# Optimization experiments

Measured on AMD Instinct MI355X. Metric: run time of the kernel, lower is better.

## Reference

```python
import jax, jax.numpy as jnp
from jax import lax
import numpy as np

IN, FC1, H = 12, 32, 16  # hard-coded dims from the module

def setup_inputs() -> dict:
    key = jax.random.key(0)
    ks = jax.random.split(key, 12)
    B, T = 4096, 512
    s = 0.1
    return {
        "x":   jax.random.normal(ks[0], (B, T, IN), dtype=jnp.float32),
        "h0":  jax.random.normal(ks[1], (1, B, H), dtype=jnp.float32),
        "c0":  jax.random.normal(ks[2], (1, B, H), dtype=jnp.float32),
        "W1":  jax.random.normal(ks[3], (FC1, IN), dtype=jnp.float32) * s,
        "b1":  jax.random.normal(ks[4], (FC1,), dtype=jnp.float32) * s,
        "W_ih": jax.random.normal(ks[5], (4 * H, FC1), dtype=jnp.float32) * s,
        "W_hh": jax.random.normal(ks[6], (4 * H, H), dtype=jnp.float32) * s,
        "b_ih": jax.random.normal(ks[7], (4 * H,), dtype=jnp.float32) * s,
        "b_hh": jax.random.normal(ks[8], (4 * H,), dtype=jnp.float32) * s,
        "W2":  jax.random.normal(ks[9], (1, H), dtype=jnp.float32) * s,
        "b2":  jax.random.normal(ks[10], (1,), dtype=jnp.float32) * s,
    }

def reference(x, h0, c0, W1, b1, W_ih, W_hh, b_ih, b_hh, W2, b2):
    # fc1 + ReLU: [B,T,12] -> [B,T,32]
    u = jnp.maximum(jnp.einsum('bti,fi->btf', x, W1) + b1, 0.0)
    # Precompute input contribution to all gates: [B,T,4H]
    xg = jnp.einsum('btf,gf->btg', u, W_ih) + (b_ih + b_hh)
    def step(carry, xg_t):
        ht, ct = carry  # [B,H]
        gates = xg_t + ht @ W_hh.T  # [B,4H]; PyTorch gate order i,f,g,o
        i, f, g, o = jnp.split(gates, 4, axis=-1)
        ct = jax.nn.sigmoid(f) * ct + jax.nn.sigmoid(i) * jnp.tanh(g)
        ht = jax.nn.sigmoid(o) * jnp.tanh(ct)
        return (ht, ct), None
    (hT, cT), _ = lax.scan(step, (h0[0], c0[0]), xg.transpose(1, 0, 2))
    # last_step of batch_first LSTM output == final hidden state hT
    out = jnp.tanh(hT @ W2.T + b2)  # [B,1]
    return out, hT[None], cT[None]
```

## Files before the change

kernel.cpp:

```cpp
#include <hip/hip_runtime.h>

typedef __fp16 f16;
typedef __attribute__((ext_vector_type(4))) __fp16 h16x4;
typedef __attribute__((ext_vector_type(4))) float f32x4;

__device__ __forceinline__ float sigm(float x) {
    return __builtin_amdgcn_rcpf(1.0f + __expf(-x));
}
__device__ __forceinline__ float tanh_fast(float x) {
    return 1.0f - 2.0f * __builtin_amdgcn_rcpf(1.0f + __expf(2.0f * x));
}
__device__ __forceinline__ h16x4 cvt4(float4 v) {
    h16x4 r; r[0] = (f16)v.x; r[1] = (f16)v.y; r[2] = (f16)v.z; r[3] = (f16)v.w;
    return r;
}
__device__ __forceinline__ h16x4 pack4(float a, float b, float c, float d) {
    auto p0 = __builtin_amdgcn_cvt_pkrtz(a, b);
    auto p1 = __builtin_amdgcn_cvt_pkrtz(c, d);
    uint2 u = make_uint2(__builtin_bit_cast(unsigned, p0),
                         __builtin_bit_cast(unsigned, p1));
    return __builtin_bit_cast(h16x4, u);
}
__device__ __forceinline__ float sel4(f32x4 v, bool q1, bool q2) {
    float a = q1 ? v[1] : v[0];
    float b = q1 ? v[3] : v[2];
    return q2 ? b : a;
}

__global__ __launch_bounds__(128) void reflex_fused(
    const float* __restrict__ x,
    const float* __restrict__ h0, const float* __restrict__ c0,
    const float* __restrict__ W1, const float* __restrict__ b1,
    const float* __restrict__ Wih, const float* __restrict__ Whh,
    const float* __restrict__ bih, const float* __restrict__ bhh,
    const float* __restrict__ W2, const float* __restrict__ b2,
    float* __restrict__ dout)
{
    const int tid = threadIdx.x;
    const int lane = tid & 63;
    const int m = lane & 15, hi = lane >> 4;
    const int b0 = blockIdx.x << 2;

    __shared__ uint2 xgl[2][1024];

    if (tid >= 64) {
        const int e = m & 3, q = m >> 2;
        const int b = b0 + e;
        h16x4 a1[2]; f32x4 c1[2];
#pragma unroll
        for (int nt = 0; nt < 2; ++nt) {
            float4 wv = make_float4(0.f, 0.f, 0.f, 0.f);
            if (hi < 3) wv = *(const float4*)(W1 + (nt * 16 + m) * 12 + 4 * hi);
            a1[nt] = cvt4(wv);
            float4 bv = *(const float4*)(b1 + nt * 16 + 4 * hi);
            c1[nt] = f32x4{bv.x, bv.y, bv.z, bv.w};
        }
        h16x4 a2[4][2];
#pragma unroll
        for (int G = 0; G < 4; ++G) {
            const int gr = G * 16 + m;
#pragma unroll
            for (int s = 0; s < 2; ++s)
                a2[G][s] = cvt4(*(const float4*)(Wih + gr * 32 + s * 16 + 4 * hi));
        }
        const int psA = q * 64 + hi * 16 + e;
        const int psB = (hi ^ q) << 2;
        const float* xrow = x + (size_t)b * 512 * 12 + 4 * hi;

        for (int F = 0; F < 32; ++F) {
            float4 bxp[4];
#pragma unroll
            for (int C = 0; C < 4; ++C)
                if (hi < 3)
                    bxp[C] = *(const float4*)(xrow + (F * 16 + C * 4 + q) * 12);
            uint2* wb = &xgl[F & 1][0];
#pragma unroll
            for (int C = 0; C < 4; ++C) {
                h16x4 bx = {0, 0, 0, 0};
                if (hi < 3) bx = cvt4(bxp[C]);
                f32x4 d0 = __builtin_amdgcn_mfma_f32_16x16x16f16(a1[0], bx, c1[0], 0, 0, 0);
                f32x4 d1 = __builtin_amdgcn_mfma_f32_16x16x16f16(a1[1], bx, c1[1], 0, 0, 0);
                h16x4 u0 = pack4(fmaxf(d0[0], 0.f), fmaxf(d0[1], 0.f),
                                 fmaxf(d0[2], 0.f), fmaxf(d0[3], 0.f));
                h16x4 u1 = pack4(fmaxf(d1[0], 0.f), fmaxf(d1[1], 0.f),
                                 fmaxf(d1[2], 0.f), fmaxf(d1[3], 0.f));
                f32x4 z4 = {0.f, 0.f, 0.f, 0.f};
                f32x4 A0 = __builtin_amdgcn_mfma_f32_16x16x16f16(a2[0][0], u0, z4, 0, 0, 0);
                f32x4 A1 = __builtin_amdgcn_mfma_f32_16x16x16f16(a2[1][0], u0, z4, 0, 0, 0);
                f32x4 A2 = __builtin_amdgcn_mfma_f32_16x16x16f16(a2[2][0], u0, z4, 0, 0, 0);
                f32x4 A3 = __builtin_amdgcn_mfma_f32_16x16x16f16(a2[3][0], u0, z4, 0, 0, 0);
                A0 = __builtin_amdgcn_mfma_f32_16x16x16f16(a2[0][1], u1, A0, 0, 0, 0);
                A1 = __builtin_amdgcn_mfma_f32_16x16x16f16(a2[1][1], u1, A1, 0, 0, 0);
                A2 = __builtin_amdgcn_mfma_f32_16x16x16f16(a2[2][1], u1, A2, 0, 0, 0);
                A3 = __builtin_amdgcn_mfma_f32_16x16x16f16(a2[3][1], u1, A3, 0, 0, 0);
#pragma unroll
                for (int r = 0; r < 4; ++r) {
                    uint2 w_;
                    auto w0 = __builtin_amdgcn_cvt_pkrtz(A0[r], A1[r]);
                    auto w1 = __builtin_amdgcn_cvt_pkrtz(A2[r], A3[r]);
                    w_.x = __builtin_bit_cast(unsigned, w0);
                    w_.y = __builtin_bit_cast(unsigned, w1);
                    wb[psA + C * 256 + (psB ^ (r << 2))] = w_;
                }
            }
            __syncthreads();
        }
    } else {
        const int e = m >> 2, q = m & 3;
        const int b = b0 + e;
        const bool q1 = (q & 1) != 0, q2 = (q & 2) != 0;

        h16x4 ar[4]; f32x4 cb[4];
#pragma unroll
        for (int G = 0; G < 4; ++G) {
            const int gr = G * 16 + m;
            ar[G] = cvt4(*(const float4*)(Whh + gr * 16 + 4 * hi));
            float4 bi = *(const float4*)(bih + G * 16 + 4 * hi);
            float4 bh = *(const float4*)(bhh + G * 16 + 4 * hi);
            cb[G] = f32x4{bi.x + bh.x, bi.y + bh.y, bi.z + bh.z, bi.w + bh.w};
        }
        h16x4 hf = cvt4(*(const float4*)(h0 + b * 16 + 4 * hi));
        float cs = c0[b * 16 + 4 * hi + q];
        float hn = 0.f;
        int va[4];
#pragma unroll
        for (int j = 0; j < 4; ++j) va[j] = hi * 16 + ((q ^ hi ^ j) << 2) + e;

#define STEP(TT, QC) do {                                                      \
    f32x4 di = __builtin_amdgcn_mfma_f32_16x16x16f16(ar[0], hf, cb[0],0,0,0);  \
    f32x4 df = __builtin_amdgcn_mfma_f32_16x16x16f16(ar[1], hf, cb[1],0,0,0);  \
    f32x4 dg = __builtin_amdgcn_mfma_f32_16x16x16f16(ar[2], hf, cb[2],0,0,0);  \
    f32x4 dq = __builtin_amdgcn_mfma_f32_16x16x16f16(ar[3], hf, cb[3],0,0,0);  \
    h16x4 gx = __builtin_bit_cast(h16x4, QC);                                  \
    if ((TT) < 14) QC = bcur[((TT) + 2) * 64 + va[((TT) + 2) & 3]];            \
    float gg = sel4(dg, q1, q2) + (float)gx[2];                                \
    float gi = sel4(di, q1, q2) + (float)gx[0];                                \
    float gf = sel4(df, q1, q2) + (float)gx[1];                                \
    float go = sel4(dq, q1, q2) + (float)gx[3];                                \
    float tg = tanh_fast(gg);                                                  \
    cs = fmaf(sigm(gf), cs, sigm(gi) * tg);                                    \
    hn = sigm(go) * tanh_fast(cs);                                             \
    int hnb = __builtin_bit_cast(int, hn);                                     \
    float j0 = __builtin_bit_cast(float,                                       \
        __builtin_amdgcn_mov_dpp(hnb, 0x00, 0xF, 0xF, true));                  \
    float j1 = __builtin_bit_cast(float,                                       \
        __builtin_amdgcn_mov_dpp(hnb, 0x55, 0xF, 0xF, true));                  \
    float j2 = __builtin_bit_cast(float,                                       \
        __builtin_amdgcn_mov_dpp(hnb, 0xAA, 0xF, 0xF, true));                  \
    float j3 = __builtin_bit_cast(float,                                       \
        __builtin_amdgcn_mov_dpp(hnb, 0xFF, 0xF, 0xF, true));                  \
    hf = pack4(j0, j1, j2, j3);                                                \
} while (0)

        __builtin_amdgcn_s_setprio(1);
        for (int T = 0; T < 32; ++T) {
            __syncthreads();
            const uint2* bcur = &xgl[T & 1][0];
            uint2 qA = bcur[va[0]];
            uint2 qB = bcur[64 + va[1]];
            STEP(0, qA);  STEP(1, qB);
            STEP(2, qA);  STEP(3, qB);
            STEP(4, qA);  STEP(5, qB);
            STEP(6, qA);  STEP(7, qB);
            STEP(8, qA);  STEP(9, qB);
            STEP(10, qA); STEP(11, qB);
            STEP(12, qA); STEP(13, qB);
            STEP(14, qA); STEP(15, qB);
        }
        __builtin_amdgcn_s_setprio(0);
#undef STEP

        dout[4096 + b * 16 + 4 * hi + q]         = hn;
        dout[4096 + 65536 + b * 16 + 4 * hi + q] = cs;
        float p = hn * W2[4 * hi + q];
        p += __shfl_xor(p, 1);
        p += __shfl_xor(p, 2);
        p += __shfl_xor(p, 16);
        p += __shfl_xor(p, 32);
        if (hi == 0 && q == 0) dout[b0 + e] = tanh_fast(p + b2[0]);
    }
}

extern "C" void kernel_launch(void* const* d_in, const int* in_sizes, int n_in,
                              void* d_out, int out_size, void* d_ws, size_t ws_size,
                              hipStream_t stream)
{
    const float* x   = (const float*)d_in[0];
    const float* h0  = (const float*)d_in[1];
    const float* c0  = (const float*)d_in[2];
    const float* W1  = (const float*)d_in[3];
    const float* b1  = (const float*)d_in[4];
    const float* Wih = (const float*)d_in[5];
    const float* Whh = (const float*)d_in[6];
    const float* bih = (const float*)d_in[7];
    const float* bhh = (const float*)d_in[8];
    const float* W2  = (const float*)d_in[9];
    const float* b2  = (const float*)d_in[10];
    float* out = (float*)d_out;

    reflex_fused<<<dim3(1024), dim3(128), 0, stream>>>(
        x, h0, c0, W1, b1, Wih, Whh, bih, bhh, W2, b2, out);
}
```

Baseline: 102.2 us.

## Stage fp32 gate pre-activations in MFMA layout to feed recurrence accumulators directly

```diff
diff --git a/kernel.cpp b/kernel.cpp
--- a/kernel.cpp
+++ b/kernel.cpp
@@ -41,7 +41,7 @@
     const int m = lane & 15, hi = lane >> 4;
     const int b0 = blockIdx.x << 2;
 
-    __shared__ uint2 xgl[2][1024];
+    __shared__ f32x4 xgl[2][1024];
 
     if (tid >= 64) {
         const int e = m & 3, q = m >> 2;
@@ -55,88 +55,100 @@
             float4 bv = *(const float4*)(b1 + nt * 16 + 4 * hi);
             c1[nt] = f32x4{bv.x, bv.y, bv.z, bv.w};
         }
-        h16x4 a2[4][2];
+        h16x4 a2[4][2]; f32x4 cbp[4];
 #pragma unroll
         for (int G = 0; G < 4; ++G) {
             const int gr = G * 16 + m;
 #pragma unroll
             for (int s = 0; s < 2; ++s)
                 a2[G][s] = cvt4(*(const float4*)(Wih + gr * 32 + s * 16 + 4 * hi));
-        }
-        const int psA = q * 64 + hi * 16 + e;
-        const int psB = (hi ^ q) << 2;
-        const float* xrow = x + (size_t)b * 512 * 12 + 4 * hi;
-
-        for (int F = 0; F < 32; ++F) {
-            float4 bxp[4];
-#pragma unroll
-            for (int C = 0; C < 4; ++C)
-                if (hi < 3)
-                    bxp[C] = *(const float4*)(xrow + (F * 16 + C * 4 + q) * 12);
-            uint2* wb = &xgl[F & 1][0];
-#pragma unroll
-            for (int C = 0; C < 4; ++C) {
-                h16x4 bx = {0, 0, 0, 0};
-                if (hi < 3) bx = cvt4(bxp[C]);
-                f32x4 d0 = __builtin_amdgcn_mfma_f32_16x16x16f16(a1[0], bx, c1[0], 0, 0, 0);
-                f32x4 d1 = __builtin_amdgcn_mfma_f32_16x16x16f16(a1[1], bx, c1[1], 0, 0, 0);
-                h16x4 u0 = pack4(fmaxf(d0[0], 0.f), fmaxf(d0[1], 0.f),
-                                 fmaxf(d0[2], 0.f), fmaxf(d0[3], 0.f));
-                h16x4 u1 = pack4(fmaxf(d1[0], 0.f), fmaxf(d1[1], 0.f),
-                                 fmaxf(d1[2], 0.f), fmaxf(d1[3], 0.f));
-                f32x4 z4 = {0.f, 0.f, 0.f, 0.f};
-                f32x4 A0 = __builtin_amdgcn_mfma_f32_16x16x16f16(a2[0][0], u0, z4, 0, 0, 0);
-                f32x4 A1 = __builtin_amdgcn_mfma_f32_16x16x16f16(a2[1][0], u0, z4, 0, 0, 0);
-                f32x4 A2 = __builtin_amdgcn_mfma_f32_16x16x16f16(a2[2][0], u0, z4, 0, 0, 0);
-                f32x4 A3 = __builtin_amdgcn_mfma_f32_16x16x16f16(a2[3][0], u0, z4, 0, 0, 0);
-                A0 = __builtin_amdgcn_mfma_f32_16x16x16f16(a2[0][1], u1, A0, 0, 0, 0);
-                A1 = __builtin_amdgcn_mfma_f32_16x16x16f16(a2[1][1], u1, A1, 0, 0, 0);
-                A2 = __builtin_amdgcn_mfma_f32_16x16x16f16(a2[2][1], u1, A2, 0, 0, 0);
-                A3 = __builtin_amdgcn_mfma_f32_16x16x16f16(a2[3][1], u1, A3, 0, 0, 0);
-#pragma unroll
-                for (int r = 0; r < 4; ++r) {
-                    uint2 w_;
-                    auto w0 = __builtin_amdgcn_cvt_pkrtz(A0[r], A1[r]);
-                    auto w1 = __builtin_amdgcn_cvt_pkrtz(A2[r], A3[r]);
-                    w_.x = __builtin_bit_cast(unsigned, w0);
-                    w_.y = __builtin_bit_cast(unsigned, w1);
-                    wb[psA + C * 256 + (psB ^ (r << 2))] = w_;
-                }
-            }
-            __syncthreads();
-        }
+            float4 bi = *(const float4*)(bih + G * 16 + 4 * hi);
+            float4 bh = *(const float4*)(bhh + G * 16 + 4 * hi);
+            cbp[G] = f32x4{bi.x + bh.x, bi.y + bh.y, bi.z + bh.z, bi.w + bh.w};
+        }
+        f32x4* pst0 = &xgl[0][q * 64 + hi * 4 + e];
+        f32x4* pst1 = &xgl[1][q * 64 + hi * 4 + e];
+        const float* xp = x + ((size_t)b * 512 + q) * 12 + 4 * hi;
+        float4 BXA[4], BXB[4];
+
+#define LOADT(BX) do {                                                         \
+    if (hi < 3) {                                                              \
+        BX[0] = *(const float4*)(xp);                                          \
+        BX[1] = *(const float4*)(xp + 48);                                     \
+        BX[2] = *(const float4*)(xp + 96);                                     \
+        BX[3] = *(const float4*)(xp + 144);                                    \
+    }                                                                          \
+    xp += 192;                                                                 \
+} while (0)
+
+#define GENSLICE(PST, BXV, CC) do {                                            \
+    h16x4 bx = {0, 0, 0, 0};                                                   \
+    if (hi < 3) bx = cvt4(BXV);                                                \
+    f32x4 d0 = __builtin_amdgcn_mfma_f32_16x16x16f16(a1[0], bx, c1[0],0,0,0);  \
+    f32x4 d1 = __builtin_amdgcn_mfma_f32_16x16x16f16(a1[1], bx, c1[1],0,0,0);  \
+    h16x4 u0 = pack4(fmaxf(d0[0],0.f), fmaxf(d0[1],0.f),                       \
+                     fmaxf(d0[2],0.f), fmaxf(d0[3],0.f));                      \
+    h16x4 u1 = pack4(fmaxf(d1[0],0.f), fmaxf(d1[1],0.f),                       \
+                     fmaxf(d1[2],0.f), fmaxf(d1[3],0.f));                      \
+    f32x4 A0 = __builtin_amdgcn_mfma_f32_16x16x16f16(a2[0][0], u0, cbp[0],0,0,0);\
+    f32x4 A1 = __builtin_amdgcn_mfma_f32_16x16x16f16(a2[1][0], u0, cbp[1],0,0,0);\
+    f32x4 A2 = __builtin_amdgcn_mfma_f32_16x16x16f16(a2[2][0], u0, cbp[2],0,0,0);\
+    f32x4 A3 = __builtin_amdgcn_mfma_f32_16x16x16f16(a2[3][0], u0, cbp[3],0,0,0);\
+    A0 = __builtin_amdgcn_mfma_f32_16x16x16f16(a2[0][1], u1, A0, 0, 0, 0);     \
+    A1 = __builtin_amdgcn_mfma_f32_16x16x16f16(a2[1][1], u1, A1, 0, 0, 0);     \
+    A2 = __builtin_amdgcn_mfma_f32_16x16x16f16(a2[2][1], u1, A2, 0, 0, 0);     \
+    A3 = __builtin_amdgcn_mfma_f32_16x16x16f16(a2[3][1], u1, A3, 0, 0, 0);     \
+    (PST)[(CC) * 256 +  0] = A0;                                               \
+    (PST)[(CC) * 256 + 16] = A1;                                               \
+    (PST)[(CC) * 256 + 32] = A2;                                               \
+    (PST)[(CC) * 256 + 48] = A3;                                               \
+} while (0)
+
+#define GENT(PST, BX) do {                                                     \
+    GENSLICE(PST, BX[0], 0); GENSLICE(PST, BX[1], 1);                          \
+    GENSLICE(PST, BX[2], 2); GENSLICE(PST, BX[3], 3);                          \
+} while (0)
+
+        LOADT(BXA);
+        for (int F2 = 0; F2 < 16; ++F2) {
+            LOADT(BXB);
+            GENT(pst0, BXA);
+            __syncthreads();
+            if (F2 < 15) LOADT(BXA);
+            GENT(pst1, BXB);
+            __syncthreads();
+        }
+#undef LOADT
+#undef GENSLICE
+#undef GENT
     } else {
         const int e = m >> 2, q = m & 3;
         const int b = b0 + e;
         const bool q1 = (q & 1) != 0, q2 = (q & 2) != 0;
 
-        h16x4 ar[4]; f32x4 cb[4];
-#pragma unroll
-        for (int G = 0; G < 4; ++G) {
-            const int gr = G * 16 + m;
-            ar[G] = cvt4(*(const float4*)(Whh + gr * 16 + 4 * hi));
-            float4 bi = *(const float4*)(bih + G * 16 + 4 * hi);
-            float4 bh = *(const float4*)(bhh + G * 16 + 4 * hi);
-            cb[G] = f32x4{bi.x + bh.x, bi.y + bh.y, bi.z + bh.z, bi.w + bh.w};
-        }
+        h16x4 ar[4];
+#pragma unroll
+        for (int G = 0; G < 4; ++G)
+            ar[G] = cvt4(*(const float4*)(Whh + (G * 16 + m) * 16 + 4 * hi));
         h16x4 hf = cvt4(*(const float4*)(h0 + b * 16 + 4 * hi));
         float cs = c0[b * 16 + 4 * hi + q];
         float hn = 0.f;
-        int va[4];
-#pragma unroll
-        for (int j = 0; j < 4; ++j) va[j] = hi * 16 + ((q ^ hi ^ j) << 2) + e;
-
-#define STEP(TT, QC) do {                                                      \
-    f32x4 di = __builtin_amdgcn_mfma_f32_16x16x16f16(ar[0], hf, cb[0],0,0,0);  \
-    f32x4 df = __builtin_amdgcn_mfma_f32_16x16x16f16(ar[1], hf, cb[1],0,0,0);  \
-    f32x4 dg = __builtin_amdgcn_mfma_f32_16x16x16f16(ar[2], hf, cb[2],0,0,0);  \
-    f32x4 dq = __builtin_amdgcn_mfma_f32_16x16x16f16(ar[3], hf, cb[3],0,0,0);  \
-    h16x4 gx = __builtin_bit_cast(h16x4, QC);                                  \
-    if ((TT) < 14) QC = bcur[((TT) + 2) * 64 + va[((TT) + 2) & 3]];            \
-    float gg = sel4(dg, q1, q2) + (float)gx[2];                                \
-    float gi = sel4(di, q1, q2) + (float)gx[0];                                \
-    float gf = sel4(df, q1, q2) + (float)gx[1];                                \
-    float go = sel4(dq, q1, q2) + (float)gx[3];                                \
+        const f32x4* ldsr = &xgl[0][0];
+        const int vbi = hi * 4 + e;
+
+#define STEP(TT, CF, OFF) do {                                                 \
+    f32x4 di = __builtin_amdgcn_mfma_f32_16x16x16f16(ar[0], hf, CF[0],0,0,0);  \
+    f32x4 df = __builtin_amdgcn_mfma_f32_16x16x16f16(ar[1], hf, CF[1],0,0,0);  \
+    f32x4 dg = __builtin_amdgcn_mfma_f32_16x16x16f16(ar[2], hf, CF[2],0,0,0);  \
+    f32x4 dq = __builtin_amdgcn_mfma_f32_16x16x16f16(ar[3], hf, CF[3],0,0,0);  \
+    if ((TT) < 14) {                                                           \
+        CF[0] = ldsr[(OFF) + ((TT) + 2) * 64 +  0 + vbi];                      \
+        CF[1] = ldsr[(OFF) + ((TT) + 2) * 64 + 16 + vbi];                      \
+        CF[2] = ldsr[(OFF) + ((TT) + 2) * 64 + 32 + vbi];                      \
+        CF[3] = ldsr[(OFF) + ((TT) + 2) * 64 + 48 + vbi];                      \
+    }                                                                          \
+    float gg = sel4(dg, q1, q2); float gi = sel4(di, q1, q2);                  \
+    float gf = sel4(df, q1, q2); float go = sel4(dq, q1, q2);                  \
     float tg = tanh_fast(gg);                                                  \
     cs = fmaf(sigm(gf), cs, sigm(gi) * tg);                                    \
     hn = sigm(go) * tanh_fast(cs);                                             \
@@ -152,23 +164,32 @@
     hf = pack4(j0, j1, j2, j3);                                                \
 } while (0)
 
+#define TILEBODY(OFF) do {                                                     \
+    f32x4 CA[4], CB[4];                                                        \
+    CA[0] = ldsr[(OFF) +  0 + vbi]; CA[1] = ldsr[(OFF) + 16 + vbi];            \
+    CA[2] = ldsr[(OFF) + 32 + vbi]; CA[3] = ldsr[(OFF) + 48 + vbi];            \
+    CB[0] = ldsr[(OFF) + 64 + vbi]; CB[1] = ldsr[(OFF) + 80 + vbi];            \
+    CB[2] = ldsr[(OFF) + 96 + vbi]; CB[3] = ldsr[(OFF) + 112 + vbi];           \
+    STEP(0, CA, OFF);  STEP(1, CB, OFF);                                       \
+    STEP(2, CA, OFF);  STEP(3, CB, OFF);                                       \
+    STEP(4, CA, OFF);  STEP(5, CB, OFF);                                       \
+    STEP(6, CA, OFF);  STEP(7, CB, OFF);                                       \
+    STEP(8, CA, OFF);  STEP(9, CB, OFF);                                       \
+    STEP(10, CA, OFF); STEP(11, CB, OFF);                                      \
+    STEP(12, CA, OFF); STEP(13, CB, OFF);                                      \
+    STEP(14, CA, OFF); STEP(15, CB, OFF);                                      \
+} while (0)
+
         __builtin_amdgcn_s_setprio(1);
-        for (int T = 0; T < 32; ++T) {
-            __syncthreads();
-            const uint2* bcur = &xgl[T & 1][0];
-            uint2 qA = bcur[va[0]];
-            uint2 qB = bcur[64 + va[1]];
-            STEP(0, qA);  STEP(1, qB);
-            STEP(2, qA);  STEP(3, qB);
-            STEP(4, qA);  STEP(5, qB);
-            STEP(6, qA);  STEP(7, qB);
-            STEP(8, qA);  STEP(9, qB);
-            STEP(10, qA); STEP(11, qB);
-            STEP(12, qA); STEP(13, qB);
-            STEP(14, qA); STEP(15, qB);
+        for (int T2 = 0; T2 < 16; ++T2) {
+            __syncthreads();
+            TILEBODY(0);
+            __syncthreads();
+            TILEBODY(1024);
         }
         __builtin_amdgcn_s_setprio(0);
 #undef STEP
+#undef TILEBODY
 
         dout[4096 + b * 16 + 4 * hi + q]         = hn;
         dout[4096 + 65536 + b * 16 + 4 * hi + q] = cs;
```

Result: no change. 101.9 us (-0.3%).
